# Performance work log

Measured on AMD Instinct MI355X. Metric: run time of the kernel, lower is better.

The kernel has to match this reference:

```python
import jax, jax.numpy as jnp
import numpy as np

EPS = 1e-09
TOP_K = 2
TEMPERATURE = 1.0


def setup_inputs() -> dict:
    key = jax.random.key(0)
    k1, k2, k3, k4 = jax.random.split(key, 4)
    B, T, H, C, E = 16, 8192, 256, 256, 16
    D = H + C          # router input dim = 512
    F = 2 * D          # hidden dim of router MLP = 1024
    inputs = jax.random.normal(k1, (B, T, H), dtype=jnp.float32)
    cond = jax.random.normal(k2, (B, T, C), dtype=jnp.float32)
    # router params (torch init: normal(0, 0.02) weights, zero bias)
    W1 = 0.02 * jax.random.normal(k3, (D, F), dtype=jnp.float32)
    b1 = jnp.zeros((F,), dtype=jnp.float32)
    W2 = 0.02 * jax.random.normal(k4, (F, E), dtype=jnp.float32)
    b2 = jnp.zeros((E,), dtype=jnp.float32)
    return {"inputs": inputs, "cond": cond, "W1": W1, "b1": b1, "W2": W2, "b2": b2}


def reference(inputs, cond, W1, b1, W2, b2):
    B, T, H = inputs.shape
    E = W2.shape[-1]
    # --- logits: concat(inputs, cond) -> Linear -> GELU(exact) -> Linear ---
    x = jnp.concatenate([inputs, cond], axis=-1).reshape(-1, H + cond.shape[-1])  # [N, D]
    h = jax.nn.gelu(x @ W1 + b1, approximate=False)                               # [N, F]
    logits = h @ W2 + b2                                                          # [N, E]
    # --- probabilities: max-subtract / temperature, softmax, clamp ---
    logits = (logits - jnp.max(logits, axis=-1, keepdims=True)) / TEMPERATURE
    probs = jax.nn.softmax(logits, axis=-1)
    probs = jnp.clip(probs, EPS, 1.0 - EPS)                                       # [N, E]
    # --- deterministic top-k selection (use_argmax / eval mode) ---
    top_vals, top_idx = jax.lax.top_k(probs, TOP_K)                               # [N, K]
    onehot = jax.nn.one_hot(top_idx, E, dtype=probs.dtype)                        # [N, K, E]
    router_mask = jnp.sum(onehot, axis=1)                                         # [N, E] 0/1
    router_probs = jnp.einsum('nke,nk->ne', onehot, top_vals)                     # scatter top-k probs
    # --- normalize selected probs ---
    router_probs = router_probs / jnp.sum(router_probs, axis=-1, keepdims=True)
    router_mask = router_mask.reshape(B, T, E)
    top_idx = top_idx.reshape(B, T, TOP_K)
    router_probs = router_probs.reshape(B, T, E)
    probs_full = probs.reshape(B, T, E)
    return (router_mask, top_idx, router_probs, probs_full)
```

## Files before the change

### kernel.cpp

```cpp
#include <hip/hip_runtime.h>
#include <math.h>

#define NTOK 131072
#define HDIM 256
#define DDIM 512
#define FDIM 1024
#define EDIM 16
#define TBLK 128
#define FCH  64
#define KST  32
#define HSS  68

#define WS_XL   134217728ULL
#define WS_W1H  268435456ULL
#define WS_W1L  269484032ULL
#define WS_NEED 270532608ULL

typedef __attribute__((ext_vector_type(8))) _Float16 v8h;
typedef __attribute__((ext_vector_type(4))) _Float16 v4h;
typedef __attribute__((ext_vector_type(4))) float v4f;

__device__ __forceinline__ void f2h2(float v, _Float16& h, _Float16& l) {
    h = (_Float16)v;
    l = (_Float16)(v - (float)h);
}

__device__ __forceinline__ void pack8(const float* u, v8h& hh, v8h& hl) {
    _Float16 h0,l0,h1,l1,h2,l2,h3,l3,h4,l4,h5,l5,h6,l6,h7,l7;
    f2h2(u[0],h0,l0); f2h2(u[1],h1,l1); f2h2(u[2],h2,l2); f2h2(u[3],h3,l3);
    f2h2(u[4],h4,l4); f2h2(u[5],h5,l5); f2h2(u[6],h6,l6); f2h2(u[7],h7,l7);
    hh[0]=h0; hh[1]=h1; hh[2]=h2; hh[3]=h3; hh[4]=h4; hh[5]=h5; hh[6]=h6; hh[7]=h7;
    hl[0]=l0; hl[1]=l1; hl[2]=l2; hl[3]=l3; hl[4]=l4; hl[5]=l5; hl[6]=l6; hl[7]=l7;
}

__global__ __launch_bounds__(256, 4)
void prep_x(const float* __restrict__ inp, const float* __restrict__ cnd,
            _Float16* __restrict__ xh, _Float16* __restrict__ xl)
{
    const size_t g = (size_t)blockIdx.x * 256 + threadIdx.x;
    const int lane = (int)(g & 63);
    const int fg   = (int)((g >> 6) & 7);
    const int T    = (int)(g >> 9);
    const int tb = T >> 4, st = T & 15;
    const int tok = tb * TBLK + fg * 16 + (lane & 15);
    const int k   = st * KST + (lane >> 4) * 8;
    const float* src = (k < HDIM) ? (inp + (size_t)tok * HDIM + k)
                                  : (cnd + (size_t)tok * HDIM + (k - HDIM));
    float u[8];
    *(float4*)&u[0] = *(const float4*)(src);
    *(float4*)&u[4] = *(const float4*)(src + 4);
    v8h hh, hl;
    pack8(u, hh, hl);
    *(v8h*)(xh + g * 8) = hh;
    *(v8h*)(xl + g * 8) = hl;
}

__global__ __launch_bounds__(256, 4)
void prep_w1(const float* __restrict__ W1,
             _Float16* __restrict__ wh, _Float16* __restrict__ wl)
{
    const int g = blockIdx.x * 256 + threadIdx.x;
    const int lane = g & 63;
    const int K = (g >> 6) & 15;
    const int F = g >> 10;
    const int f  = F * 16 + (lane & 15);
    const int kb = K * KST + (lane >> 4) * 8;
    float u[8];
#pragma unroll
    for (int e = 0; e < 8; ++e)
        u[e] = W1[(size_t)(kb + e) * FDIM + f];
    v8h hh, hl;
    pack8(u, hh, hl);
    *(v8h*)(wh + (size_t)g * 8) = hh;
    *(v8h*)(wl + (size_t)g * 8) = hl;
}

__global__ __launch_bounds__(256, 2)
void router_mfma10(const _Float16* __restrict__ xh, const _Float16* __restrict__ xl,
                   const _Float16* __restrict__ w1h, const _Float16* __restrict__ w1l,
                   const float* __restrict__ b1,
                   const float* __restrict__ W2,
                   const float* __restrict__ b2,
                   float* __restrict__ out)
{
    __shared__ __align__(16) char smem[34816];
    _Float16* xs_h = (_Float16*)(smem);
    _Float16* xs_l = (_Float16*)(smem + 8192);
    _Float16* ws_h = (_Float16*)(smem + 16384);
    _Float16* ws_l = (_Float16*)(smem + 20480);
    _Float16* hs_h = (_Float16*)(smem);
    _Float16* hs_l = (_Float16*)(smem + 17408);

    const int tid  = threadIdx.x;
    const int lane = tid & 63;
    const int w    = tid >> 6;
    const int wr   = w >> 1;
    const int wc   = w & 1;
    const int l15  = lane & 15;
    const int l4   = lane >> 4;
    const int t0   = blockIdx.x * TBLK;

    const float b2v = b2[l15];
    v4f accL[2] = {{0.f,0.f,0.f,0.f},{0.f,0.f,0.f,0.f}};

    for (int fc = 0; fc < FDIM; fc += FCH) {
        v4f acc[4][2];
#pragma unroll
        for (int mf = 0; mf < 4; ++mf)
#pragma unroll
            for (int nf = 0; nf < 2; ++nf)
                acc[mf][nf] = (v4f){0.f,0.f,0.f,0.f};

        for (int st = 0; st < 16; ++st) {
            __syncthreads();
            {
                const v8h* sh = (const v8h*)(xh + ((size_t)blockIdx.x * 16 + st) * 4096);
                const v8h* sl = (const v8h*)(xl + ((size_t)blockIdx.x * 16 + st) * 4096);
                ((v8h*)xs_h)[tid]       = sh[tid];
                ((v8h*)xs_h)[tid + 256] = sh[tid + 256];
                ((v8h*)xs_l)[tid]       = sl[tid];
                ((v8h*)xs_l)[tid + 256] = sl[tid + 256];
            }
            {
                const size_t wb = (((size_t)((fc >> 4) + (tid >> 6)) * 16 + st) * 64
                                   + (tid & 63)) * 8;
                ((v8h*)ws_h)[tid] = *(const v8h*)(w1h + wb);
                ((v8h*)ws_l)[tid] = *(const v8h*)(w1l + wb);
            }
            __syncthreads();
            {
                v8h bh[2], bl[2];
#pragma unroll
                for (int nf = 0; nf < 2; ++nf) {
                    const int off = ((2 * wc + nf) * 64 + lane) * 8;
                    bh[nf] = *(const v8h*)(ws_h + off);
                    bl[nf] = *(const v8h*)(ws_l + off);
                }
#pragma unroll
                for (int mf = 0; mf < 4; ++mf) {
                    const int aoff = ((4 * wr + mf) * 64 + lane) * 8;
                    const v8h ah = *(const v8h*)(xs_h + aoff);
                    const v8h al = *(const v8h*)(xs_l + aoff);
#pragma unroll
                    for (int nf = 0; nf < 2; ++nf) {
                        acc[mf][nf] = __builtin_amdgcn_mfma_f32_16x16x32_f16(ah, bh[nf], acc[mf][nf], 0, 0, 0);
                        acc[mf][nf] = __builtin_amdgcn_mfma_f32_16x16x32_f16(al, bh[nf], acc[mf][nf], 0, 0, 0);
                        acc[mf][nf] = __builtin_amdgcn_mfma_f32_16x16x32_f16(ah, bl[nf], acc[mf][nf], 0, 0, 0);
                    }
                }
            }
        }
        __syncthreads();

        {
            float b1v[2];
#pragma unroll
            for (int nf = 0; nf < 2; ++nf)
                b1v[nf] = b1[fc + 32 * wc + 16 * nf + l15];
#pragma unroll
            for (int mf = 0; mf < 4; ++mf)
#pragma unroll
                for (int nf = 0; nf < 2; ++nf)
#pragma unroll
                    for (int r = 0; r < 4; ++r) {
                        const float v = acc[mf][nf][r] + b1v[nf];
                        const float gl = 0.5f * v * (1.0f + erff(v * 0.70710678118654752f));
                        _Float16 hh, hl;
                        f2h2(gl, hh, hl);
                        const int tok  = 64 * wr + 16 * mf + 4 * l4 + r;
                        const int fcol = 32 * wc + 16 * nf + l15;
                        hs_h[tok * HSS + fcol] = hh;
                        hs_l[tok * HSS + fcol] = hl;
                    }
        }
        __syncthreads();

#pragma unroll
        for (int ks = 0; ks < 2; ++ks) {
            v8h vbh, vbl;
#pragma unroll
            for (int j = 0; j < 8; ++j) {
                const float u = W2[(size_t)(fc + 32 * ks + 8 * l4 + j) * EDIM + l15];
                _Float16 hh, hl;
                f2h2(u, hh, hl);
                vbh[j] = hh; vbl[j] = hl;
            }
#pragma unroll
            for (int mf2 = 0; mf2 < 2; ++mf2) {
                const int aoff = (32 * w + 16 * mf2 + l15) * HSS + 32 * ks + 8 * l4;
                const v8h vah = *(const v8h*)(hs_h + aoff);
                const v8h val = *(const v8h*)(hs_l + aoff);
                accL[mf2] = __builtin_amdgcn_mfma_f32_16x16x32_f16(vah, vbh, accL[mf2], 0, 0, 0);
                accL[mf2] = __builtin_amdgcn_mfma_f32_16x16x32_f16(val, vbh, accL[mf2], 0, 0, 0);
                accL[mf2] = __builtin_amdgcn_mfma_f32_16x16x32_f16(vah, vbl, accL[mf2], 0, 0, 0);
            }
        }
    }

    float lg[8];
#pragma unroll
    for (int mf2 = 0; mf2 < 2; ++mf2)
#pragma unroll
        for (int r = 0; r < 4; ++r)
            lg[mf2 * 4 + r] = accL[mf2][r] + b2v;

    const int tx = l15;
#pragma unroll
    for (int i = 0; i < 8; ++i) {
        const int t = t0 + 32 * w + 16 * (i >> 2) + 4 * l4 + (i & 3);
        float mx = lg[i];
#pragma unroll
        for (int m = 1; m < 16; m <<= 1) mx = fmaxf(mx, __shfl_xor(mx, m, 64));
        float p = expf(lg[i] - mx);
        float s = p;
#pragma unroll
        for (int m = 1; m < 16; m <<= 1) s += __shfl_xor(s, m, 64);
        float pr = p / s;
        pr = fminf(fmaxf(pr, 1e-9f), 1.0f - 1e-9f);

        float v1 = pr; int i1 = tx;
#pragma unroll
        for (int m = 1; m < 16; m <<= 1) {
            const float vo = __shfl_xor(v1, m, 64);
            const int   io = __shfl_xor(i1, m, 64);
            if (vo > v1 || (vo == v1 && io < i1)) { v1 = vo; i1 = io; }
        }
        float v2 = (tx == i1) ? -1.0f : pr; int i2 = tx;
#pragma unroll
        for (int m = 1; m < 16; m <<= 1) {
            const float vo = __shfl_xor(v2, m, 64);
            const int   io = __shfl_xor(i2, m, 64);
            if (vo > v2 || (vo == v2 && io < i2)) { v2 = vo; i2 = io; }
        }
        const float rs = 1.0f / (v1 + v2);

        float* om  = out + (size_t)t * EDIM;
        float* orp = out + (size_t)NTOK * 18 + (size_t)t * EDIM;
        float* opf = out + (size_t)NTOK * 34 + (size_t)t * EDIM;
        om[tx]  = (tx == i1 || tx == i2) ? 1.0f : 0.0f;
        orp[tx] = (tx == i1) ? v1 * rs : ((tx == i2) ? v2 * rs : 0.0f);
        opf[tx] = pr;
        if (tx == 0) {
            float2* oi = (float2*)(out + (size_t)NTOK * 16 + (size_t)t * 2);
            *oi = make_float2((float)i1, (float)i2);
        }
    }
}

#define XST  40
#define HST  68
__global__ __launch_bounds__(256, 2)
void router_mfma7(const float* __restrict__ inp,
                  const float* __restrict__ cnd,
                  const float* __restrict__ W1,
                  const float* __restrict__ b1,
                  const float* __restrict__ W2,
                  const float* __restrict__ b2,
                  float* __restrict__ out)
{
    __shared__ __align__(16) char smem[34816];
    _Float16* xs_h = (_Float16*)(smem);
    _Float16* xs_l = (_Float16*)(smem + 10240);
    _Float16* ws_h = (_Float16*)(smem + 20480);
    _Float16* ws_l = (_Float16*)(smem + 25600);
    float*    hs   = (float*)(smem);

    const int tid  = threadIdx.x;
    const int lane = tid & 63;
    const int w    = tid >> 6;
    const int wr   = w >> 1;
    const int wc   = w & 1;
    const int l15  = lane & 15;
    const int l4   = lane >> 4;
    const int t0   = blockIdx.x * TBLK;
    const int ty   = tid >> 4;
    const int tx   = tid & 15;
    const int kq   = tid & 7;
    const int xr   = tid >> 3;
    const int fcl  = tid & 63;
    const int kg   = tid >> 6;

    float lg[8];
    { const float bb = b2[tx];
#pragma unroll
      for (int i = 0; i < 8; ++i) lg[i] = bb; }

    for (int fc = 0; fc < FDIM; fc += FCH) {
        v4f acc[4][2];
#pragma unroll
        for (int mf = 0; mf < 4; ++mf)
#pragma unroll
            for (int nf = 0; nf < 2; ++nf) acc[mf][nf] = (v4f){0.f,0.f,0.f,0.f};

        for (int st = 0; st < 16; ++st) {
            const int kc = st * KST;
            __syncthreads();
            {
                const float* src = (kc < HDIM) ? (inp + (size_t)t0 * HDIM + kc)
                                               : (cnd + (size_t)t0 * HDIM + (kc - HDIM));
#pragma unroll
                for (int p = 0; p < 4; ++p) {
                    const int row = xr + 32 * p;
                    const float4 v = *(const float4*)(src + (size_t)row * HDIM + kq * 4);
                    _Float16 h0,l0,h1,l1,h2,l2,h3,l3;
                    f2h2(v.x,h0,l0); f2h2(v.y,h1,l1); f2h2(v.z,h2,l2); f2h2(v.w,h3,l3);
                    v4h hh, hl;
                    hh[0]=h0; hh[1]=h1; hh[2]=h2; hh[3]=h3;
                    hl[0]=l0; hl[1]=l1; hl[2]=l2; hl[3]=l3;
                    *(v4h*)(xs_h + row * XST + kq * 4) = hh;
                    *(v4h*)(xs_l + row * XST + kq * 4) = hl;
                }
            }
#pragma unroll
            for (int s = 0; s < 2; ++s) {
                const int kb = 4 * kg + 16 * s;
                const float u0 = W1[(size_t)(kc + kb + 0) * FDIM + fc + fcl];
                const float u1 = W1[(size_t)(kc + kb + 1) * FDIM + fc + fcl];
                const float u2 = W1[(size_t)(kc + kb + 2) * FDIM + fc + fcl];
                const float u3 = W1[(size_t)(kc + kb + 3) * FDIM + fc + fcl];
                _Float16 h0,l0,h1,l1,h2,l2,h3,l3;
                f2h2(u0,h0,l0); f2h2(u1,h1,l1); f2h2(u2,h2,l2); f2h2(u3,h3,l3);
                v4h hh, hl;
                hh[0]=h0; hh[1]=h1; hh[2]=h2; hh[3]=h3;
                hl[0]=l0; hl[1]=l1; hl[2]=l2; hl[3]=l3;
                *(v4h*)(ws_h + fcl * XST + kb) = hh;
                *(v4h*)(ws_l + fcl * XST + kb) = hl;
            }
            __syncthreads();
            {
                v8h bh[2], bl[2];
#pragma unroll
                for (int nf = 0; nf < 2; ++nf) {
                    const int off = (32 * wc + 16 * nf + l15) * XST + 8 * l4;
                    bh[nf] = *(const v8h*)(ws_h + off);
                    bl[nf] = *(const v8h*)(ws_l + off);
                }
#pragma unroll
                for (int mf = 0; mf < 4; ++mf) {
                    const int off = (64 * wr + 16 * mf + l15) * XST + 8 * l4;
                    const v8h ah = *(const v8h*)(xs_h + off);
                    const v8h al = *(const v8h*)(xs_l + off);
#pragma unroll
                    for (int nf = 0; nf < 2; ++nf) {
                        acc[mf][nf] = __builtin_amdgcn_mfma_f32_16x16x32_f16(ah, bh[nf], acc[mf][nf], 0, 0, 0);
                        acc[mf][nf] = __builtin_amdgcn_mfma_f32_16x16x32_f16(al, bh[nf], acc[mf][nf], 0, 0, 0);
                        acc[mf][nf] = __builtin_amdgcn_mfma_f32_16x16x32_f16(ah, bl[nf], acc[mf][nf], 0, 0, 0);
                    }
                }
            }
        }
        __syncthreads();
        {
            float b1v[2];
#pragma unroll
            for (int nf = 0; nf < 2; ++nf) b1v[nf] = b1[fc + 32 * wc + 16 * nf + l15];
#pragma unroll
            for (int mf = 0; mf < 4; ++mf)
#pragma unroll
                for (int nf = 0; nf < 2; ++nf)
#pragma unroll
                    for (int r = 0; r < 4; ++r) {
                        const float v = acc[mf][nf][r] + b1v[nf];
                        const int tok  = 64 * wr + 16 * mf + 4 * l4 + r;
                        const int fcol = 32 * wc + 16 * nf + l15;
                        hs[tok * HST + fcol] = 0.5f * v * (1.0f + erff(v * 0.70710678118654752f));
                    }
        }
        __syncthreads();
#pragma unroll
        for (int jb = 0; jb < 16; ++jb) {
            const int jbs = (jb + 4 * l4) & 15;
            float w2v[4];
#pragma unroll
            for (int j = 0; j < 4; ++j)
                w2v[j] = W2[(size_t)(fc + jbs * 4 + j) * EDIM + tx];
#pragma unroll
            for (int i = 0; i < 8; ++i) {
                const float4 hv = *(const float4*)(hs + (ty * 8 + i) * HST + jbs * 4);
                lg[i] = fmaf(hv.x, w2v[0], lg[i]);
                lg[i] = fmaf(hv.y, w2v[1], lg[i]);
                lg[i] = fmaf(hv.z, w2v[2], lg[i]);
                lg[i] = fmaf(hv.w, w2v[3], lg[i]);
            }
        }
    }
#pragma unroll
    for (int i = 0; i < 8; ++i) {
        const int t = t0 + ty * 8 + i;
        float mx = lg[i];
#pragma unroll
        for (int m = 1; m < 16; m <<= 1) mx = fmaxf(mx, __shfl_xor(mx, m, 64));
        float p = expf(lg[i] - mx);
        float s = p;
#pragma unroll
        for (int m = 1; m < 16; m <<= 1) s += __shfl_xor(s, m, 64);
        float pr = p / s;
        pr = fminf(fmaxf(pr, 1e-9f), 1.0f - 1e-9f);
        float v1 = pr; int i1 = tx;
#pragma unroll
        for (int m = 1; m < 16; m <<= 1) {
            const float vo = __shfl_xor(v1, m, 64);
            const int   io = __shfl_xor(i1, m, 64);
            if (vo > v1 || (vo == v1 && io < i1)) { v1 = vo; i1 = io; }
        }
        float v2 = (tx == i1) ? -1.0f : pr; int i2 = tx;
#pragma unroll
        for (int m = 1; m < 16; m <<= 1) {
            const float vo = __shfl_xor(v2, m, 64);
            const int   io = __shfl_xor(i2, m, 64);
            if (vo > v2 || (vo == v2 && io < i2)) { v2 = vo; i2 = io; }
        }
        const float rs = 1.0f / (v1 + v2);
        float* om  = out + (size_t)t * EDIM;
        float* orp = out + (size_t)NTOK * 18 + (size_t)t * EDIM;
        float* opf = out + (size_t)NTOK * 34 + (size_t)t * EDIM;
        om[tx]  = (tx == i1 || tx == i2) ? 1.0f : 0.0f;
        orp[tx] = (tx == i1) ? v1 * rs : ((tx == i2) ? v2 * rs : 0.0f);
        opf[tx] = pr;
        if (tx == 0) {
            float2* oi = (float2*)(out + (size_t)NTOK * 16 + (size_t)t * 2);
            *oi = make_float2((float)i1, (float)i2);
        }
    }
}

extern "C" void kernel_launch(void* const* d_in, const int* in_sizes, int n_in,
                              void* d_out, int out_size, void* d_ws, size_t ws_size,
                              hipStream_t stream)
{
    const float* inp = (const float*)d_in[0];
    const float* cnd = (const float*)d_in[1];
    const float* W1  = (const float*)d_in[2];
    const float* b1  = (const float*)d_in[3];
    const float* W2  = (const float*)d_in[4];
    const float* b2  = (const float*)d_in[5];
    float* out = (float*)d_out;

    if (ws_size >= WS_NEED) {
        char* wsb = (char*)d_ws;
        _Float16* xh  = (_Float16*)(wsb);
        _Float16* xl  = (_Float16*)(wsb + WS_XL);
        _Float16* w1h = (_Float16*)(wsb + WS_W1H);
        _Float16* w1l = (_Float16*)(wsb + WS_W1L);
        hipLaunchKernelGGL(prep_x, dim3(32768), dim3(256), 0, stream, inp, cnd, xh, xl);
        hipLaunchKernelGGL(prep_w1, dim3(256), dim3(256), 0, stream, W1, w1h, w1l);
        hipLaunchKernelGGL(router_mfma10, dim3(NTOK / TBLK), dim3(256), 0, stream,
                           xh, xl, w1h, w1l, b1, W2, b2, out);
    } else {
        hipLaunchKernelGGL(router_mfma7, dim3(NTOK / TBLK), dim3(256), 0, stream,
                           inp, cnd, W1, b1, W2, b2, out);
    }
}
```

Baseline: 751.2 us.

## Widen hidden chunk to 128 so X tiles are reused across more columns

Doubles the F chunk processed per pass over the token tile from 64 to 128, so the pre-split fp16 X tile is streamed from global memory half as many times. Each wave now computes a 64x64 accumulator block (16 MFMA tiles) instead of 64x32. The GELU and second-GEMM stage is done in two halves that share the existing hidden-state shared-memory buffer, with extra barriers between them. This doubles the accumulator registers per wave, which risks spills or lower occupancy under the 2-blocks launch bound, and adds synchronisation in the epilogue.

```diff
diff --git a/kernel.cpp b/kernel.cpp
--- a/kernel.cpp
+++ b/kernel.cpp
@@ -7,7 +7,7 @@
 #define FDIM 1024
 #define EDIM 16
 #define TBLK 128
-#define FCH  64
+#define FCH  128
 #define KST  32
 #define HSS  68
 
@@ -76,7 +76,7 @@
 }
 
 __global__ __launch_bounds__(256, 2)
-void router_mfma10(const _Float16* __restrict__ xh, const _Float16* __restrict__ xl,
+void router_mfma11(const _Float16* __restrict__ xh, const _Float16* __restrict__ xl,
                    const _Float16* __restrict__ w1h, const _Float16* __restrict__ w1l,
                    const float* __restrict__ b1,
                    const float* __restrict__ W2,
@@ -87,7 +87,7 @@
     _Float16* xs_h = (_Float16*)(smem);
     _Float16* xs_l = (_Float16*)(smem + 8192);
     _Float16* ws_h = (_Float16*)(smem + 16384);
-    _Float16* ws_l = (_Float16*)(smem + 20480);
+    _Float16* ws_l = (_Float16*)(smem + 24576);
     _Float16* hs_h = (_Float16*)(smem);
     _Float16* hs_l = (_Float16*)(smem + 17408);
 
@@ -95,7 +95,7 @@
     const int lane = tid & 63;
     const int w    = tid >> 6;
     const int wr   = w >> 1;
-    const int wc   = w & 1;
+    const int wf   = w & 1;
     const int l15  = lane & 15;
     const int l4   = lane >> 4;
     const int t0   = blockIdx.x * TBLK;
@@ -104,11 +104,11 @@
     v4f accL[2] = {{0.f,0.f,0.f,0.f},{0.f,0.f,0.f,0.f}};
 
     for (int fc = 0; fc < FDIM; fc += FCH) {
-        v4f acc[4][2];
+        v4f acc[4][4];
 #pragma unroll
         for (int mf = 0; mf < 4; ++mf)
 #pragma unroll
-            for (int nf = 0; nf < 2; ++nf)
+            for (int nf = 0; nf < 4; ++nf)
                 acc[mf][nf] = (v4f){0.f,0.f,0.f,0.f};
 
         for (int st = 0; st < 16; ++st) {
@@ -122,78 +122,86 @@
                 ((v8h*)xs_l)[tid + 256] = sl[tid + 256];
             }
             {
-                const size_t wb = (((size_t)((fc >> 4) + (tid >> 6)) * 16 + st) * 64
-                                   + (tid & 63)) * 8;
-                ((v8h*)ws_h)[tid] = *(const v8h*)(w1h + wb);
-                ((v8h*)ws_l)[tid] = *(const v8h*)(w1l + wb);
+                const int fr0 = tid >> 6;
+                const size_t wb0 = (((size_t)((fc >> 4) + fr0) * 16 + st) * 64 + (tid & 63)) * 8;
+                const size_t wb1 = (((size_t)((fc >> 4) + 4 + fr0) * 16 + st) * 64 + (tid & 63)) * 8;
+                ((v8h*)ws_h)[tid]       = *(const v8h*)(w1h + wb0);
+                ((v8h*)ws_h)[tid + 256] = *(const v8h*)(w1h + wb1);
+                ((v8h*)ws_l)[tid]       = *(const v8h*)(w1l + wb0);
+                ((v8h*)ws_l)[tid + 256] = *(const v8h*)(w1l + wb1);
             }
             __syncthreads();
-            {
-                v8h bh[2], bl[2];
-#pragma unroll
-                for (int nf = 0; nf < 2; ++nf) {
-                    const int off = ((2 * wc + nf) * 64 + lane) * 8;
-                    bh[nf] = *(const v8h*)(ws_h + off);
-                    bl[nf] = *(const v8h*)(ws_l + off);
-                }
-#pragma unroll
-                for (int mf = 0; mf < 4; ++mf) {
-                    const int aoff = ((4 * wr + mf) * 64 + lane) * 8;
-                    const v8h ah = *(const v8h*)(xs_h + aoff);
-                    const v8h al = *(const v8h*)(xs_l + aoff);
-#pragma unroll
-                    for (int nf = 0; nf < 2; ++nf) {
-                        acc[mf][nf] = __builtin_amdgcn_mfma_f32_16x16x32_f16(ah, bh[nf], acc[mf][nf], 0, 0, 0);
-                        acc[mf][nf] = __builtin_amdgcn_mfma_f32_16x16x32_f16(al, bh[nf], acc[mf][nf], 0, 0, 0);
-                        acc[mf][nf] = __builtin_amdgcn_mfma_f32_16x16x32_f16(ah, bl[nf], acc[mf][nf], 0, 0, 0);
+#pragma unroll
+            for (int mg = 0; mg < 2; ++mg) {
+                v8h ah[2], al[2];
+#pragma unroll
+                for (int q = 0; q < 2; ++q) {
+                    const int aoff = ((4 * wr + 2 * mg + q) * 64 + lane) * 8;
+                    ah[q] = *(const v8h*)(xs_h + aoff);
+                    al[q] = *(const v8h*)(xs_l + aoff);
+                }
+#pragma unroll
+                for (int nf = 0; nf < 4; ++nf) {
+                    const int boff = ((4 * wf + nf) * 64 + lane) * 8;
+                    const v8h bh = *(const v8h*)(ws_h + boff);
+                    const v8h bl = *(const v8h*)(ws_l + boff);
+#pragma unroll
+                    for (int q = 0; q < 2; ++q) {
+                        acc[2*mg+q][nf] = __builtin_amdgcn_mfma_f32_16x16x32_f16(ah[q], bh, acc[2*mg+q][nf], 0, 0, 0);
+                        acc[2*mg+q][nf] = __builtin_amdgcn_mfma_f32_16x16x32_f16(al[q], bh, acc[2*mg+q][nf], 0, 0, 0);
+                        acc[2*mg+q][nf] = __builtin_amdgcn_mfma_f32_16x16x32_f16(ah[q], bl, acc[2*mg+q][nf], 0, 0, 0);
                     }
                 }
             }
         }
         __syncthreads();
 
-        {
-            float b1v[2];
-#pragma unroll
-            for (int nf = 0; nf < 2; ++nf)
-                b1v[nf] = b1[fc + 32 * wc + 16 * nf + l15];
-#pragma unroll
-            for (int mf = 0; mf < 4; ++mf)
-#pragma unroll
-                for (int nf = 0; nf < 2; ++nf)
-#pragma unroll
-                    for (int r = 0; r < 4; ++r) {
-                        const float v = acc[mf][nf][r] + b1v[nf];
-                        const float gl = 0.5f * v * (1.0f + erff(v * 0.70710678118654752f));
-                        _Float16 hh, hl;
-                        f2h2(gl, hh, hl);
-                        const int tok  = 64 * wr + 16 * mf + 4 * l4 + r;
-                        const int fcol = 32 * wc + 16 * nf + l15;
-                        hs_h[tok * HSS + fcol] = hh;
-                        hs_l[tok * HSS + fcol] = hl;
-                    }
-        }
-        __syncthreads();
-
-#pragma unroll
-        for (int ks = 0; ks < 2; ++ks) {
-            v8h vbh, vbl;
-#pragma unroll
-            for (int j = 0; j < 8; ++j) {
-                const float u = W2[(size_t)(fc + 32 * ks + 8 * l4 + j) * EDIM + l15];
-                _Float16 hh, hl;
-                f2h2(u, hh, hl);
-                vbh[j] = hh; vbl[j] = hl;
-            }
-#pragma unroll
-            for (int mf2 = 0; mf2 < 2; ++mf2) {
-                const int aoff = (32 * w + 16 * mf2 + l15) * HSS + 32 * ks + 8 * l4;
-                const v8h vah = *(const v8h*)(hs_h + aoff);
-                const v8h val = *(const v8h*)(hs_l + aoff);
-                accL[mf2] = __builtin_amdgcn_mfma_f32_16x16x32_f16(vah, vbh, accL[mf2], 0, 0, 0);
-                accL[mf2] = __builtin_amdgcn_mfma_f32_16x16x32_f16(val, vbh, accL[mf2], 0, 0, 0);
-                accL[mf2] = __builtin_amdgcn_mfma_f32_16x16x32_f16(vah, vbl, accL[mf2], 0, 0, 0);
-            }
+        float b1v[4];
+#pragma unroll
+        for (int nf = 0; nf < 4; ++nf)
+            b1v[nf] = b1[fc + 64 * wf + 16 * nf + l15];
+
+#pragma unroll
+        for (int h = 0; h < 2; ++h) {
+            if (wf == h) {
+#pragma unroll
+                for (int mf = 0; mf < 4; ++mf)
+#pragma unroll
+                    for (int nf = 0; nf < 4; ++nf)
+#pragma unroll
+                        for (int r = 0; r < 4; ++r) {
+                            const float v = acc[mf][nf][r] + b1v[nf];
+                            const float gl = 0.5f * v * (1.0f + erff(v * 0.70710678118654752f));
+                            _Float16 hh, hl;
+                            f2h2(gl, hh, hl);
+                            const int tok  = 64 * wr + 16 * mf + 4 * l4 + r;
+                            const int fcol = 16 * nf + l15;
+                            hs_h[tok * HSS + fcol] = hh;
+                            hs_l[tok * HSS + fcol] = hl;
+                        }
+            }
+            __syncthreads();
+#pragma unroll
+            for (int ks = 0; ks < 2; ++ks) {
+                v8h vbh, vbl;
+#pragma unroll
+                for (int j = 0; j < 8; ++j) {
+                    const float u = W2[(size_t)(fc + 64 * h + 32 * ks + 8 * l4 + j) * EDIM + l15];
+                    _Float16 hh, hl;
+                    f2h2(u, hh, hl);
+                    vbh[j] = hh; vbl[j] = hl;
+                }
+#pragma unroll
+                for (int mf2 = 0; mf2 < 2; ++mf2) {
+                    const int aoff = (32 * w + 16 * mf2 + l15) * HSS + 32 * ks + 8 * l4;
+                    const v8h vah = *(const v8h*)(hs_h + aoff);
+                    const v8h val = *(const v8h*)(hs_l + aoff);
+                    accL[mf2] = __builtin_amdgcn_mfma_f32_16x16x32_f16(vah, vbh, accL[mf2], 0, 0, 0);
+                    accL[mf2] = __builtin_amdgcn_mfma_f32_16x16x32_f16(val, vbh, accL[mf2], 0, 0, 0);
+                    accL[mf2] = __builtin_amdgcn_mfma_f32_16x16x32_f16(vah, vbl, accL[mf2], 0, 0, 0);
+                }
+            }
+            if (h == 0) __syncthreads();
         }
     }
 
@@ -249,6 +257,7 @@
 
 #define XST  40
 #define HST  68
+#define FCHB 64
 __global__ __launch_bounds__(256, 2)
 void router_mfma7(const float* __restrict__ inp,
                   const float* __restrict__ cnd,
@@ -285,7 +294,7 @@
 #pragma unroll
       for (int i = 0; i < 8; ++i) lg[i] = bb; }
 
-    for (int fc = 0; fc < FDIM; fc += FCH) {
+    for (int fc = 0; fc < FDIM; fc += FCHB) {
         v4f acc[4][2];
 #pragma unroll
         for (int mf = 0; mf < 4; ++mf)
@@ -444,7 +453,7 @@
         _Float16* w1l = (_Float16*)(wsb + WS_W1L);
         hipLaunchKernelGGL(prep_x, dim3(32768), dim3(256), 0, stream, inp, cnd, xh, xl);
         hipLaunchKernelGGL(prep_w1, dim3(256), dim3(256), 0, stream, W1, w1h, w1l);
-        hipLaunchKernelGGL(router_mfma10, dim3(NTOK / TBLK), dim3(256), 0, stream,
+        hipLaunchKernelGGL(router_mfma11, dim3(NTOK / TBLK), dim3(256), 0, stream,
                            xh, xl, w1h, w1l, b1, W2, b2, out);
     } else {
         hipLaunchKernelGGL(router_mfma7, dim3(NTOK / TBLK), dim3(256), 0, stream,
```

Measured after the change: 688.1 us. 1.09x faster.
